# Kernel optimization log

Hardware: AMD Instinct MI355X
Metric: run time of the kernel (lower is better)

Reference implementation:

```python
import jax, jax.numpy as jnp
import numpy as np

N_NODES = 50000
N_EDGES = 800000
F_IN = 128
HEADS = 4
HEAD_DIM = 32  # hidden_size // heads
HIDDEN = HEADS * HEAD_DIM
N_GRAPHS = 64
LEAKY_SLOPE = 0.01
EPS_LN = 1e-5


def setup_inputs() -> dict:
    key = jax.random.key(0)
    ks = jax.random.split(key, 12)
    x = jax.random.normal(ks[0], (N_NODES, F_IN), dtype=jnp.float32)
    edge_index = jax.random.randint(ks[1], (2, N_EDGES), 0, N_NODES, dtype=jnp.int64)
    batch = jnp.sort(jax.random.randint(ks[2], (N_NODES,), 0, N_GRAPHS, dtype=jnp.int64))
    s = 1.0 / np.sqrt(F_IN).astype(np.float32)
    Wq = jax.random.normal(ks[3], (F_IN, HIDDEN), dtype=jnp.float32) * s
    bq = jnp.zeros((HIDDEN,), jnp.float32)
    Wk = jax.random.normal(ks[4], (F_IN, HIDDEN), dtype=jnp.float32) * s
    bk = jnp.zeros((HIDDEN,), jnp.float32)
    Wv = jax.random.normal(ks[5], (F_IN, HIDDEN), dtype=jnp.float32) * s
    bv = jnp.zeros((HIDDEN,), jnp.float32)
    Ws = jax.random.normal(ks[6], (F_IN, HIDDEN), dtype=jnp.float32) * s  # root/skip lin
    bs = jnp.zeros((HIDDEN,), jnp.float32)
    ln_w = jnp.ones((HIDDEN,), jnp.float32)
    ln_b = jnp.zeros((HIDDEN,), jnp.float32)
    return {"x": x, "edge_index": edge_index, "batch": batch,
            "Wq": Wq, "bq": bq, "Wk": Wk, "bk": bk, "Wv": Wv, "bv": bv,
            "Ws": Ws, "bs": bs, "ln_w": ln_w, "ln_b": ln_b}


def reference(x, edge_index, batch, Wq, bq, Wk, bk, Wv, bv, Ws, bs, ln_w, ln_b):
    N = x.shape[0]
    src, dst = edge_index[0], edge_index[1]  # message j(src) -> i(dst)
    q = (x @ Wq + bq).reshape(N, HEADS, HEAD_DIM)
    k = (x @ Wk + bk).reshape(N, HEADS, HEAD_DIM)
    v = (x @ Wv + bv).reshape(N, HEADS, HEAD_DIM)
    # per-edge attention logits [E, H]
    alpha = jnp.einsum('ehc,ehc->eh', q[dst], k[src]) / jnp.sqrt(jnp.float32(HEAD_DIM))
    # scatter-softmax over incoming edges of each destination node
    m = jax.ops.segment_max(alpha, dst, num_segments=N)
    m = jnp.where(jnp.isfinite(m), m, 0.0)  # empty segments -> -inf; neutralize
    ex = jnp.exp(alpha - m[dst])
    denom = jax.ops.segment_sum(ex, dst, num_segments=N)
    attn = ex / (denom[dst] + 1e-16)
    # scatter-add aggregation of weighted values, concat heads
    out = jax.ops.segment_sum(attn[:, :, None] * v[src], dst, num_segments=N)
    out = out.reshape(N, HIDDEN) + x @ Ws + bs  # root/skip connection
    # PyG graph-mode LayerNorm: normalize over all nodes+channels of each graph
    cnt = jax.ops.segment_sum(jnp.ones((N,), out.dtype), batch, num_segments=N_GRAPHS)
    norm = jnp.maximum(cnt, 1.0) * HIDDEN
    mean = jax.ops.segment_sum(out.sum(-1), batch, num_segments=N_GRAPHS) / norm
    outc = out - mean[batch][:, None]
    var = jax.ops.segment_sum((outc * outc).sum(-1), batch, num_segments=N_GRAPHS) / norm
    y = outc / jnp.sqrt(var + EPS_LN)[batch][:, None]
    y = y * ln_w + ln_b
    y = jnp.where(y > 0, y, LEAKY_SLOPE * y)  # LeakyReLU
    return (y, attn)
```

## Files before the change

### kernel.cpp

```cpp
#include <hip/hip_runtime.h>
#include <hip/hip_fp16.h>

constexpr int N_NODES = 50000;
constexpr int N_EDGES = 800000;
constexpr int HIDDEN  = 128;
constexpr float RSQRT_D = 0.17677669529663687f;
constexpr int Y_SIZE = N_NODES * HIDDEN;
constexpr int M_PAD  = 50048;
constexpr int SCAN_BLOCKS = 196;
constexpr int XCVT_BLOCKS = (M_PAD * 16) / 256;

constexpr size_t OFF_Q      = 0;
constexpr size_t OFF_K      = 6400000;
constexpr size_t OFF_V      = 12800000;
constexpr size_t OFF_S      = 19200000;
constexpr size_t OFF_DENOM  = 25600000;
constexpr size_t OFF_GSUM   = 25800000;
constexpr size_t OFF_GSQ    = 25800064;
constexpr size_t OFF_GCNT   = 25800128;
constexpr size_t OFF_DEG    = 25800192;
constexpr size_t OFF_OFFS   = 25850192;
constexpr size_t OFF_CURSOR = 25900224;
constexpr size_t OFF_CSR    = 25950224;
constexpr size_t OFF_PART   = 27550224;

typedef __attribute__((ext_vector_type(8))) short bf16x8;
typedef __attribute__((ext_vector_type(4))) float f32x4;

__device__ __forceinline__ short f2bf(float f) {
    unsigned u = __float_as_uint(f);
    unsigned r = (u + 0x7fff + ((u >> 16) & 1)) >> 16;
    return (short)r;
}

__device__ __forceinline__ void gload_lds16(const void* g, void* l) {
    __builtin_amdgcn_global_load_lds(
        (const __attribute__((address_space(1))) void*)g,
        (__attribute__((address_space(3))) void*)l, 16, 0, 0);
}

__global__ __launch_bounds__(256) void k_cvt(
    const float* __restrict__ x,
    const float* __restrict__ Wq, const float* __restrict__ Wk,
    const float* __restrict__ Wv, const float* __restrict__ Wsm,
    short* __restrict__ xs, short* __restrict__ wt)
{
    int b = blockIdx.x;
    if (b < XCVT_BLOCKS) {
        int tid = b * 256 + threadIdx.x;
        int row = tid >> 4, ci = tid & 15;
        short o[8];
        if (row < N_NODES) {
            float4 a = *(const float4*)&x[(size_t)row * 128 + ci * 8];
            float4 bb = *(const float4*)&x[(size_t)row * 128 + ci * 8 + 4];
            o[0] = f2bf(a.x); o[1] = f2bf(a.y); o[2] = f2bf(a.z); o[3] = f2bf(a.w);
            o[4] = f2bf(bb.x); o[5] = f2bf(bb.y); o[6] = f2bf(bb.z); o[7] = f2bf(bb.w);
        } else {
            #pragma unroll
            for (int j = 0; j < 8; ++j) o[j] = 0;
        }
        int cs = ci ^ (row & 7);
        *(int4*)&xs[(size_t)row * 128 + cs * 8] = *(int4*)o;
    } else {
        int tid = (b - XCVT_BLOCKS) * 256 + threadIdx.x;
        int mat = tid >> 11, n = (tid >> 4) & 127, kg = tid & 15;
        const float* W = (mat == 0) ? Wq : (mat == 1) ? Wk : (mat == 2) ? Wv : Wsm;
        short o[8];
        #pragma unroll
        for (int j = 0; j < 8; ++j) o[j] = f2bf(W[(kg * 8 + j) * 128 + n]);
        int cs = kg ^ (n & 7);
        *(int4*)&wt[mat * 16384 + n * 128 + cs * 8] = *(int4*)o;
    }
}

__global__ __launch_bounds__(256) void k_mm(
    const short* __restrict__ xs, const short* __restrict__ wt,
    const float* __restrict__ bq, const float* __restrict__ bk,
    const float* __restrict__ bv, const float* __restrict__ bs,
    __half* __restrict__ q, __half* __restrict__ kb,
    __half* __restrict__ vb, float* __restrict__ s)
{
    __shared__ __align__(16) char As[32768];
    __shared__ __align__(16) char Bs[32768];
    const int t = threadIdx.x, lane = t & 63, wv = t >> 6;
    const int m0 = blockIdx.x * 128;
    const int wm = wv >> 1, wn = wv & 1;

    const char* gA = (const char*)xs + (size_t)m0 * 256;
    #pragma unroll
    for (int i = 0; i < 8; ++i) {
        int chunk = wv * 8 + i;
        gload_lds16(gA + chunk * 1024 + lane * 16, As + chunk * 1024);
        gload_lds16((const char*)wt + chunk * 1024 + lane * 16, Bs + chunk * 1024);
    }
    __syncthreads();

    bf16x8 af[4][4];
    #pragma unroll
    for (int ks = 0; ks < 4; ++ks) {
        const int cbase = ks * 64 + ((lane >> 4) << 4);
        #pragma unroll
        for (int mf = 0; mf < 4; ++mf) {
            int mr = wm * 64 + mf * 16 + (lane & 15);
            af[ks][mf] = *(const bf16x8*)(As + mr * 256 + (cbase ^ ((mr & 7) << 4)));
        }
    }

    const float* Bbs[4] = {bq, bk, bv, bs};
    #pragma unroll
    for (int mat = 0; mat < 4; ++mat) {
        f32x4 acc[4][4];
        #pragma unroll
        for (int nf = 0; nf < 4; ++nf) {
            float bc = Bbs[mat][wn * 64 + nf * 16 + (lane & 15)];
            #pragma unroll
            for (int mf = 0; mf < 4; ++mf) acc[mf][nf] = (f32x4){bc, bc, bc, bc};
        }
        #pragma unroll
        for (int ks = 0; ks < 4; ++ks) {
            bf16x8 bfr[4];
            const int cbase = ks * 64 + ((lane >> 4) << 4);
            #pragma unroll
            for (int nf = 0; nf < 4; ++nf) {
                int nc = wn * 64 + nf * 16 + (lane & 15);
                bfr[nf] = *(const bf16x8*)(Bs + nc * 256 + (cbase ^ ((nc & 7) << 4)));
            }
            #pragma unroll
            for (int mf = 0; mf < 4; ++mf)
                #pragma unroll
                for (int nf = 0; nf < 4; ++nf)
                    acc[mf][nf] = __builtin_amdgcn_mfma_f32_16x16x32_bf16(
                        af[ks][mf], bfr[nf], acc[mf][nf], 0, 0, 0);
        }
        __syncthreads();
        if (mat < 3) {
            const char* gB = (const char*)wt + (mat + 1) * 32768;
            #pragma unroll
            for (int i = 0; i < 8; ++i) {
                int chunk = wv * 8 + i;
                gload_lds16(gB + chunk * 1024 + lane * 16, Bs + chunk * 1024);
            }
        }
        const int colbase = wn * 64 + (lane & 15);
        if (mat == 3) {
            #pragma unroll
            for (int mf = 0; mf < 4; ++mf) {
                int rowb = m0 + wm * 64 + mf * 16 + ((lane >> 4) << 2);
                #pragma unroll
                for (int nf = 0; nf < 4; ++nf) {
                    int col = colbase + nf * 16;
                    #pragma unroll
                    for (int r = 0; r < 4; ++r) {
                        int node = rowb + r;
                        if (node < N_NODES) s[(size_t)node * 128 + col] = acc[mf][nf][r];
                    }
                }
            }
        } else {
            __half* O = (mat == 0) ? q : (mat == 1) ? kb : vb;
            #pragma unroll
            for (int mf = 0; mf < 4; ++mf) {
                int rowb = m0 + wm * 64 + mf * 16 + ((lane >> 4) << 2);
                #pragma unroll
                for (int nf = 0; nf < 4; ++nf) {
                    int col = colbase + nf * 16;
                    #pragma unroll
                    for (int r = 0; r < 4; ++r) {
                        int node = rowb + r;
                        if (node < N_NODES)
                            O[(size_t)node * 128 + col] = __float2half_rn(acc[mf][nf][r]);
                    }
                }
            }
        }
        __syncthreads();
    }
}

__global__ __launch_bounds__(256) void k_hist(const int* __restrict__ dst,
                                              int* __restrict__ deg)
{
    int e = blockIdx.x * 256 + threadIdx.x;
    atomicAdd(&deg[dst[e]], 1);
}

__global__ __launch_bounds__(256) void k_scan1(const int* __restrict__ deg,
                                               int* __restrict__ part)
{
    const int t = threadIdx.x;
    int idx = blockIdx.x * 256 + t;
    int v = (idx < N_NODES) ? deg[idx] : 0;
    #pragma unroll
    for (int o = 1; o < 64; o <<= 1) v += __shfl_xor(v, o);
    __shared__ int wsum[4];
    if ((t & 63) == 0) wsum[t >> 6] = v;
    __syncthreads();
    if (t == 0) part[blockIdx.x] = wsum[0] + wsum[1] + wsum[2] + wsum[3];
}

__global__ __launch_bounds__(256) void k_scan2(int* __restrict__ part)
{
    __shared__ int buf[256];
    const int t = threadIdx.x;
    int v = (t < SCAN_BLOCKS) ? part[t] : 0;
    buf[t] = v;
    __syncthreads();
    for (int o = 1; o < 256; o <<= 1) {
        int tmp = (t >= o) ? buf[t - o] : 0;
        __syncthreads();
        buf[t] += tmp;
        __syncthreads();
    }
    if (t < SCAN_BLOCKS) part[t] = buf[t] - v;
}

__global__ __launch_bounds__(256) void k_scan3(const int* __restrict__ deg,
                                               const int* __restrict__ part,
                                               int* __restrict__ offs,
                                               int* __restrict__ cursor)
{
    const int t = threadIdx.x;
    const int idx = blockIdx.x * 256 + t;
    const int lane = t & 63, w = t >> 6;
    int v = (idx < N_NODES) ? deg[idx] : 0;
    int inc = v;
    #pragma unroll
    for (int o = 1; o < 64; o <<= 1) {
        int nb = __shfl_up(inc, o);
        if (lane >= o) inc += nb;
    }
    __shared__ int wsum[4];
    if (lane == 63) wsum[w] = inc;
    __syncthreads();
    int wbase = 0;
    #pragma unroll
    for (int i = 0; i < 4; ++i) if (i < w) wbase += wsum[i];
    int excl = part[blockIdx.x] + wbase + inc - v;
    if (idx < N_NODES) {
        offs[idx] = excl;
        cursor[idx] = excl;
    }
    if (idx == 0) offs[N_NODES] = N_EDGES;
}

__global__ __launch_bounds__(256) void k_scatter(
    const int* __restrict__ src, const int* __restrict__ dst,
    int* __restrict__ cursor, int2* __restrict__ csr)
{
    int e = blockIdx.x * 256 + threadIdx.x;
    int d = dst[e];
    int pos = atomicAdd(&cursor[d], 1);
    csr[pos] = make_int2(src[e], e);
}

__global__ __launch_bounds__(256) void k_fused(
    const __half2* __restrict__ qb, const __half2* __restrict__ kb,
    const __half2* __restrict__ vb, const float* __restrict__ s,
    const int* __restrict__ offs, const int2* __restrict__ csr,
    float* __restrict__ exbuf, float* __restrict__ denom,
    float* __restrict__ outb)
{
    const int t = threadIdx.x;
    const int lane = t & 63;
    const int n = blockIdx.x * 4 + (t >> 6);
    const int begin = offs[n], end = offs[n + 1];
    const float2 qv = __half22float2(qb[(size_t)n * 64 + lane]);
    const float2 sv = *(const float2*)&s[(size_t)n * 128 + lane * 2];
    const int h = lane >> 4;
    float acc0 = 0.f, acc1 = 0.f, dsum = 0.f;
    int i = begin;
    for (; i + 8 <= end; i += 8) {
        int2 c[8];
        #pragma unroll
        for (int u = 0; u < 8; ++u) c[u] = csr[i + u];
        __half2 kh[8], vh[8];
        #pragma unroll
        for (int u = 0; u < 8; ++u) kh[u] = kb[(size_t)c[u].x * 64 + lane];
        #pragma unroll
        for (int u = 0; u < 8; ++u) vh[u] = vb[(size_t)c[u].x * 64 + lane];
        float p[8];
        #pragma unroll
        for (int u = 0; u < 8; ++u) {
            float2 kf = __half22float2(kh[u]);
            p[u] = qv.x * kf.x + qv.y * kf.y;
        }
        #pragma unroll
        for (int u = 0; u < 8; ++u) p[u] += __shfl_xor(p[u], 1);
        #pragma unroll
        for (int u = 0; u < 8; ++u) p[u] += __shfl_xor(p[u], 2);
        #pragma unroll
        for (int u = 0; u < 8; ++u) p[u] += __shfl_xor(p[u], 4);
        #pragma unroll
        for (int u = 0; u < 8; ++u) p[u] += __shfl_xor(p[u], 8);
        #pragma unroll
        for (int u = 0; u < 8; ++u) {
            float ex = __expf(p[u] * RSQRT_D);
            dsum += ex;
            float2 vf = __half22float2(vh[u]);
            acc0 += ex * vf.x;
            acc1 += ex * vf.y;
            if ((lane & 15) == 0) exbuf[c[u].y * 4 + h] = ex;
        }
    }
    for (; i < end; ++i) {
        const int2 c0 = csr[i];
        const __half2 kh0 = kb[(size_t)c0.x * 64 + lane];
        const __half2 vh0 = vb[(size_t)c0.x * 64 + lane];
        const float2 k0 = __half22float2(kh0);
        float p0 = qv.x * k0.x + qv.y * k0.y;
        p0 += __shfl_xor(p0, 1);
        p0 += __shfl_xor(p0, 2);
        p0 += __shfl_xor(p0, 4);
        p0 += __shfl_xor(p0, 8);
        const float ex0 = __expf(p0 * RSQRT_D);
        dsum += ex0;
        const float2 v0 = __half22float2(vh0);
        acc0 += ex0 * v0.x;
        acc1 += ex0 * v0.y;
        if ((lane & 15) == 0) exbuf[c0.y * 4 + h] = ex0;
    }
    if ((lane & 15) == 0) denom[n * 4 + h] = dsum;
    const float rdn = 1.f / (dsum + 1e-16f);
    float2 o = make_float2(acc0 * rdn + sv.x, acc1 * rdn + sv.y);
    *(float2*)&outb[(size_t)n * 128 + lane * 2] = o;
}

__global__ __launch_bounds__(256) void k_norm(
    float* __restrict__ attn, const float* __restrict__ denom,
    const int* __restrict__ dst)
{
    int idx = blockIdx.x * 256 + threadIdx.x;
    int e = idx >> 2, h = idx & 3;
    attn[idx] = attn[idx] / (denom[dst[e] * 4 + h] + 1e-16f);
}

__global__ __launch_bounds__(256) void k_stats(
    const float* __restrict__ out, const int* __restrict__ batch,
    float* __restrict__ gsum, float* __restrict__ gsq, int* __restrict__ gcnt)
{
    __shared__ float nsum[32], nsq[32];
    __shared__ int   ngr[32];
    const int t = threadIdx.x;
    const int nl = t >> 3, part = t & 7;
    const int n = blockIdx.x * 32 + nl;
    float lsum = 0.f, lsq = 0.f;
    if (n < N_NODES) {
        size_t base = (size_t)n * 128 + part * 16;
        #pragma unroll
        for (int i = 0; i < 4; ++i) {
            float4 o = *(const float4*)&out[base + i * 4];
            lsum += o.x + o.y + o.z + o.w;
            lsq  += o.x * o.x + o.y * o.y + o.z * o.z + o.w * o.w;
        }
    }
    #pragma unroll
    for (int o = 1; o < 8; o <<= 1) {
        lsum += __shfl_xor(lsum, o);
        lsq  += __shfl_xor(lsq, o);
    }
    if (part == 0) { nsum[nl] = lsum; nsq[nl] = lsq; ngr[nl] = (n < N_NODES) ? batch[n] : -1; }
    __syncthreads();
    if (t == 0) {
        float acc = 0.f, accq = 0.f; int cg = ngr[0], cnt = 0;
        for (int i = 0; i < 32; ++i) {
            int g = ngr[i];
            if (g != cg) {
                if (cg >= 0) { atomicAdd(&gsum[cg], acc); atomicAdd(&gsq[cg], accq);
                               atomicAdd(&gcnt[cg], cnt); }
                acc = 0.f; accq = 0.f; cnt = 0; cg = g;
            }
            acc += nsum[i]; accq += nsq[i]; ++cnt;
        }
        if (cg >= 0) { atomicAdd(&gsum[cg], acc); atomicAdd(&gsq[cg], accq);
                       atomicAdd(&gcnt[cg], cnt); }
    }
}

__global__ __launch_bounds__(256) void k_final(
    const float* __restrict__ out, const int* __restrict__ batch,
    const float* __restrict__ gsum, const float* __restrict__ gsq,
    const int* __restrict__ gcnt,
    const float* __restrict__ lnw, const float* __restrict__ lnb,
    float* __restrict__ y)
{
    int idx = blockIdx.x * 256 + threadIdx.x;
    int n = idx >> 7, c = idx & 127;
    int g = batch[n];
    float norm = fmaxf((float)gcnt[g], 1.f) * 128.f;
    float mean = gsum[g] / norm;
    float var  = gsq[g] / norm - mean * mean;
    float inv  = rsqrtf(var + 1e-5f);
    float val  = (out[idx] - mean) * inv * lnw[c] + lnb[c];
    y[idx] = val > 0.f ? val : 0.01f * val;
}

extern "C" void kernel_launch(void* const* d_in, const int* in_sizes, int n_in,
                              void* d_out, int out_size, void* d_ws, size_t ws_size,
                              hipStream_t stream)
{
    (void)in_sizes; (void)n_in; (void)out_size; (void)ws_size;
    const float* x    = (const float*)d_in[0];
    const int*   ei   = (const int*)  d_in[1];
    const int*   batch= (const int*)  d_in[2];
    const float* Wq   = (const float*)d_in[3];
    const float* bq   = (const float*)d_in[4];
    const float* Wk   = (const float*)d_in[5];
    const float* bk   = (const float*)d_in[6];
    const float* Wv   = (const float*)d_in[7];
    const float* bv   = (const float*)d_in[8];
    const float* Wsm  = (const float*)d_in[9];
    const float* bs   = (const float*)d_in[10];
    const float* lnw  = (const float*)d_in[11];
    const float* lnb  = (const float*)d_in[12];

    float* outp = (float*)d_out;
    float* ws   = (float*)d_ws;

    const int* srcI = ei;
    const int* dstI = ei + N_EDGES;

    __half* qb      = (__half*)(ws + OFF_Q);
    __half* kb      = (__half*)(ws + OFF_K);
    __half* vb      = (__half*)(ws + OFF_V);
    float*  s       = ws + OFF_S;
    float*  denom   = ws + OFF_DENOM;
    short*  wt      = (short*)(ws + OFF_DENOM);
    float*  gsum    = ws + OFF_GSUM;
    float*  gsq     = ws + OFF_GSQ;
    int*    gcnt    = (int*)(ws + OFF_GCNT);
    int*    deg     = (int*)(ws + OFF_DEG);
    int*    offs    = (int*)(ws + OFF_OFFS);
    int*    cursor  = (int*)(ws + OFF_CURSOR);
    int2*   csr     = (int2*)(ws + OFF_CSR);
    int*    partArr = (int*)(ws + OFF_PART);

    float* outb  = outp;
    short* x_swz = (short*)outp;
    float* attn  = outp + Y_SIZE;

    hipMemsetAsync(gsum, 0, (size_t)(192 + N_NODES) * sizeof(float), stream);

    k_cvt<<<XCVT_BLOCKS + 32, 256, 0, stream>>>(x, Wq, Wk, Wv, Wsm, x_swz, wt);
    k_mm<<<M_PAD / 128, 256, 0, stream>>>(x_swz, wt, bq, bk, bv, bs, qb, kb, vb, s);

    k_hist<<<N_EDGES / 256, 256, 0, stream>>>(dstI, deg);
    k_scan1<<<SCAN_BLOCKS, 256, 0, stream>>>(deg, partArr);
    k_scan2<<<1, 256, 0, stream>>>(partArr);
    k_scan3<<<SCAN_BLOCKS, 256, 0, stream>>>(deg, partArr, offs, cursor);
    k_scatter<<<N_EDGES / 256, 256, 0, stream>>>(srcI, dstI, cursor, csr);
    k_fused<<<N_NODES / 4, 256, 0, stream>>>((const __half2*)qb, (const __half2*)kb,
                                             (const __half2*)vb, s, offs, csr,
                                             attn, denom, outb);
    k_norm<<<(N_EDGES * 4) / 256, 256, 0, stream>>>(attn, denom, dstI);
    k_stats<<<(N_NODES + 31) / 32, 256, 0, stream>>>(outb, batch, gsum, gsq, gcnt);
    k_final<<<Y_SIZE / 256, 256, 0, stream>>>(outb, batch, gsum, gsq, gcnt,
                                              lnw, lnb, outp);
}
```

Before: 266.3 us.

## Interleave K/V rows, store skip in fp16, fuse histogram into prep kernel

K and V projections are now written interleaved per node (256 halves per row), so the edge gather reads both from one contiguous 512-byte region. The skip projection is stored as fp16 instead of fp32, halving its traffic. The degree histogram moves into the conversion kernel, saving a launch, and the edge loop unroll drops from 8 to 4. The fp16 skip output adds rounding error to the result.

```diff
diff --git a/kernel.cpp b/kernel.cpp
--- a/kernel.cpp
+++ b/kernel.cpp
@@ -9,6 +9,7 @@
 constexpr int M_PAD  = 50048;
 constexpr int SCAN_BLOCKS = 196;
 constexpr int XCVT_BLOCKS = (M_PAD * 16) / 256;
+constexpr int HIST_BLOCKS = N_EDGES / 256;
 
 constexpr size_t OFF_Q      = 0;
 constexpr size_t OFF_K      = 6400000;
@@ -39,11 +40,12 @@
         (__attribute__((address_space(3))) void*)l, 16, 0, 0);
 }
 
-__global__ __launch_bounds__(256) void k_cvt(
+__global__ __launch_bounds__(256) void k_prep(
     const float* __restrict__ x,
     const float* __restrict__ Wq, const float* __restrict__ Wk,
     const float* __restrict__ Wv, const float* __restrict__ Wsm,
-    short* __restrict__ xs, short* __restrict__ wt)
+    const int* __restrict__ dst,
+    short* __restrict__ xs, short* __restrict__ wt, int* __restrict__ deg)
 {
     int b = blockIdx.x;
     if (b < XCVT_BLOCKS) {
@@ -61,7 +63,7 @@
         }
         int cs = ci ^ (row & 7);
         *(int4*)&xs[(size_t)row * 128 + cs * 8] = *(int4*)o;
-    } else {
+    } else if (b < XCVT_BLOCKS + 32) {
         int tid = (b - XCVT_BLOCKS) * 256 + threadIdx.x;
         int mat = tid >> 11, n = (tid >> 4) & 127, kg = tid & 15;
         const float* W = (mat == 0) ? Wq : (mat == 1) ? Wk : (mat == 2) ? Wv : Wsm;
@@ -70,6 +72,9 @@
         for (int j = 0; j < 8; ++j) o[j] = f2bf(W[(kg * 8 + j) * 128 + n]);
         int cs = kg ^ (n & 7);
         *(int4*)&wt[mat * 16384 + n * 128 + cs * 8] = *(int4*)o;
+    } else {
+        int e = (b - XCVT_BLOCKS - 32) * 256 + threadIdx.x;
+        atomicAdd(&deg[dst[e]], 1);
     }
 }
 
@@ -77,8 +82,7 @@
     const short* __restrict__ xs, const short* __restrict__ wt,
     const float* __restrict__ bq, const float* __restrict__ bk,
     const float* __restrict__ bv, const float* __restrict__ bs,
-    __half* __restrict__ q, __half* __restrict__ kb,
-    __half* __restrict__ vb, float* __restrict__ s)
+    __half* __restrict__ qb, __half* __restrict__ kv, __half* __restrict__ sb)
 {
     __shared__ __align__(16) char As[32768];
     __shared__ __align__(16) char Bs[32768];
@@ -141,47 +145,25 @@
                 gload_lds16(gB + chunk * 1024 + lane * 16, Bs + chunk * 1024);
             }
         }
+        __half* base = (mat == 0) ? qb : (mat == 1) ? kv : (mat == 2) ? (kv + 128) : sb;
+        const int rs = (mat == 1 || mat == 2) ? 256 : 128;
         const int colbase = wn * 64 + (lane & 15);
-        if (mat == 3) {
-            #pragma unroll
-            for (int mf = 0; mf < 4; ++mf) {
-                int rowb = m0 + wm * 64 + mf * 16 + ((lane >> 4) << 2);
+        #pragma unroll
+        for (int mf = 0; mf < 4; ++mf) {
+            int rowb = m0 + wm * 64 + mf * 16 + ((lane >> 4) << 2);
+            #pragma unroll
+            for (int nf = 0; nf < 4; ++nf) {
+                int col = colbase + nf * 16;
                 #pragma unroll
-                for (int nf = 0; nf < 4; ++nf) {
-                    int col = colbase + nf * 16;
-                    #pragma unroll
-                    for (int r = 0; r < 4; ++r) {
-                        int node = rowb + r;
-                        if (node < N_NODES) s[(size_t)node * 128 + col] = acc[mf][nf][r];
-                    }
+                for (int r = 0; r < 4; ++r) {
+                    int node = rowb + r;
+                    if (node < N_NODES)
+                        base[(size_t)node * rs + col] = __float2half_rn(acc[mf][nf][r]);
                 }
             }
-        } else {
-            __half* O = (mat == 0) ? q : (mat == 1) ? kb : vb;
-            #pragma unroll
-            for (int mf = 0; mf < 4; ++mf) {
-                int rowb = m0 + wm * 64 + mf * 16 + ((lane >> 4) << 2);
-                #pragma unroll
-                for (int nf = 0; nf < 4; ++nf) {
-                    int col = colbase + nf * 16;
-                    #pragma unroll
-                    for (int r = 0; r < 4; ++r) {
-                        int node = rowb + r;
-                        if (node < N_NODES)
-                            O[(size_t)node * 128 + col] = __float2half_rn(acc[mf][nf][r]);
-                    }
-                }
-            }
         }
         __syncthreads();
     }
-}
-
-__global__ __launch_bounds__(256) void k_hist(const int* __restrict__ dst,
-                                              int* __restrict__ deg)
-{
-    int e = blockIdx.x * 256 + threadIdx.x;
-    atomicAdd(&deg[dst[e]], 1);
 }
 
 __global__ __launch_bounds__(256) void k_scan1(const int* __restrict__ deg,
@@ -254,8 +236,8 @@
 }
 
 __global__ __launch_bounds__(256) void k_fused(
-    const __half2* __restrict__ qb, const __half2* __restrict__ kb,
-    const __half2* __restrict__ vb, const float* __restrict__ s,
+    const __half2* __restrict__ qb, const __half2* __restrict__ kvp,
+    const __half2* __restrict__ sb,
     const int* __restrict__ offs, const int2* __restrict__ csr,
     float* __restrict__ exbuf, float* __restrict__ denom,
     float* __restrict__ outb)
@@ -265,35 +247,35 @@
     const int n = blockIdx.x * 4 + (t >> 6);
     const int begin = offs[n], end = offs[n + 1];
     const float2 qv = __half22float2(qb[(size_t)n * 64 + lane]);
-    const float2 sv = *(const float2*)&s[(size_t)n * 128 + lane * 2];
+    const float2 sv = __half22float2(sb[(size_t)n * 64 + lane]);
     const int h = lane >> 4;
     float acc0 = 0.f, acc1 = 0.f, dsum = 0.f;
     int i = begin;
-    for (; i + 8 <= end; i += 8) {
-        int2 c[8];
-        #pragma unroll
-        for (int u = 0; u < 8; ++u) c[u] = csr[i + u];
-        __half2 kh[8], vh[8];
-        #pragma unroll
-        for (int u = 0; u < 8; ++u) kh[u] = kb[(size_t)c[u].x * 64 + lane];
-        #pragma unroll
-        for (int u = 0; u < 8; ++u) vh[u] = vb[(size_t)c[u].x * 64 + lane];
-        float p[8];
-        #pragma unroll
-        for (int u = 0; u < 8; ++u) {
+    for (; i + 4 <= end; i += 4) {
+        int2 c[4];
+        #pragma unroll
+        for (int u = 0; u < 4; ++u) c[u] = csr[i + u];
+        __half2 kh[4], vh[4];
+        #pragma unroll
+        for (int u = 0; u < 4; ++u) kh[u] = kvp[(size_t)c[u].x * 128 + lane];
+        #pragma unroll
+        for (int u = 0; u < 4; ++u) vh[u] = kvp[(size_t)c[u].x * 128 + 64 + lane];
+        float p[4];
+        #pragma unroll
+        for (int u = 0; u < 4; ++u) {
             float2 kf = __half22float2(kh[u]);
             p[u] = qv.x * kf.x + qv.y * kf.y;
         }
         #pragma unroll
-        for (int u = 0; u < 8; ++u) p[u] += __shfl_xor(p[u], 1);
-        #pragma unroll
-        for (int u = 0; u < 8; ++u) p[u] += __shfl_xor(p[u], 2);
-        #pragma unroll
-        for (int u = 0; u < 8; ++u) p[u] += __shfl_xor(p[u], 4);
-        #pragma unroll
-        for (int u = 0; u < 8; ++u) p[u] += __shfl_xor(p[u], 8);
-        #pragma unroll
-        for (int u = 0; u < 8; ++u) {
+        for (int u = 0; u < 4; ++u) p[u] += __shfl_xor(p[u], 1);
+        #pragma unroll
+        for (int u = 0; u < 4; ++u) p[u] += __shfl_xor(p[u], 2);
+        #pragma unroll
+        for (int u = 0; u < 4; ++u) p[u] += __shfl_xor(p[u], 4);
+        #pragma unroll
+        for (int u = 0; u < 4; ++u) p[u] += __shfl_xor(p[u], 8);
+        #pragma unroll
+        for (int u = 0; u < 4; ++u) {
             float ex = __expf(p[u] * RSQRT_D);
             dsum += ex;
             float2 vf = __half22float2(vh[u]);
@@ -304,8 +286,8 @@
     }
     for (; i < end; ++i) {
         const int2 c0 = csr[i];
-        const __half2 kh0 = kb[(size_t)c0.x * 64 + lane];
-        const __half2 vh0 = vb[(size_t)c0.x * 64 + lane];
+        const __half2 kh0 = kvp[(size_t)c0.x * 128 + lane];
+        const __half2 vh0 = kvp[(size_t)c0.x * 128 + 64 + lane];
         const float2 k0 = __half22float2(kh0);
         float p0 = qv.x * k0.x + qv.y * k0.y;
         p0 += __shfl_xor(p0, 1);
@@ -420,9 +402,8 @@
     const int* dstI = ei + N_EDGES;
 
     __half* qb      = (__half*)(ws + OFF_Q);
-    __half* kb      = (__half*)(ws + OFF_K);
-    __half* vb      = (__half*)(ws + OFF_V);
-    float*  s       = ws + OFF_S;
+    __half* kv      = (__half*)(ws + OFF_K);
+    __half* sb      = (__half*)(ws + OFF_S);
     float*  denom   = ws + OFF_DENOM;
     short*  wt      = (short*)(ws + OFF_DENOM);
     float*  gsum    = ws + OFF_GSUM;
@@ -440,16 +421,16 @@
 
     hipMemsetAsync(gsum, 0, (size_t)(192 + N_NODES) * sizeof(float), stream);
 
-    k_cvt<<<XCVT_BLOCKS + 32, 256, 0, stream>>>(x, Wq, Wk, Wv, Wsm, x_swz, wt);
-    k_mm<<<M_PAD / 128, 256, 0, stream>>>(x_swz, wt, bq, bk, bv, bs, qb, kb, vb, s);
-
-    k_hist<<<N_EDGES / 256, 256, 0, stream>>>(dstI, deg);
+    k_prep<<<XCVT_BLOCKS + 32 + HIST_BLOCKS, 256, 0, stream>>>(
+        x, Wq, Wk, Wv, Wsm, dstI, x_swz, wt, deg);
+    k_mm<<<M_PAD / 128, 256, 0, stream>>>(x_swz, wt, bq, bk, bv, bs, qb, kv, sb);
+
     k_scan1<<<SCAN_BLOCKS, 256, 0, stream>>>(deg, partArr);
     k_scan2<<<1, 256, 0, stream>>>(partArr);
     k_scan3<<<SCAN_BLOCKS, 256, 0, stream>>>(deg, partArr, offs, cursor);
     k_scatter<<<N_EDGES / 256, 256, 0, stream>>>(srcI, dstI, cursor, csr);
-    k_fused<<<N_NODES / 4, 256, 0, stream>>>((const __half2*)qb, (const __half2*)kb,
-                                             (const __half2*)vb, s, offs, csr,
+    k_fused<<<N_NODES / 4, 256, 0, stream>>>((const __half2*)qb, (const __half2*)kv,
+                                             (const __half2*)sb, offs, csr,
                                              attn, denom, outb);
     k_norm<<<(N_EDGES * 4) / 256, 256, 0, stream>>>(attn, denom, dstI);
     k_stats<<<(N_NODES + 31) / 32, 256, 0, stream>>>(outb, batch, gsum, gsq, gcnt);
```

Result: faster. 240.3 us (-9.8%).
